# Kernel optimization log

Measured on AMD Instinct MI355X. Metric: run time of the kernel, lower is better.

The kernel has to match this reference:

```python
import jax, jax.numpy as jnp
import numpy as np

B, N, NC, DIM, H, D, M, TOPK = 1, 2048, 2048, 1024, 16, 64, 16, 64


def _l2norm(t):
    # F.normalize(t, p=2, dim=-1)
    return t / jnp.clip(jnp.linalg.norm(t, axis=-1, keepdims=True), 1e-12)


def _attn_layer(x, ctx, q_mask, k_mask, Wq, Wk, Wv, th_pre, th_post,
                mem_k, mem_v, scale_p, hs, Wo):
    b, n, _ = x.shape
    h, m, d = mem_k.shape
    nc = ctx.shape[1]
    q = (x @ Wq).reshape(b, n, h, d).transpose(0, 2, 1, 3)      # b h i d
    k = (ctx @ Wk).reshape(b, nc, h, d).transpose(0, 2, 1, 3)   # b h j d
    v = (ctx @ Wv).reshape(b, nc, h, d).transpose(0, 2, 1, 3)
    # memory key/values prepended
    k = jnp.concatenate([jnp.broadcast_to(mem_k[None], (b, h, m, d)), k], axis=2)
    v = jnp.concatenate([jnp.broadcast_to(mem_v[None], (b, h, m, d)), v], axis=2)
    # input mask (q_mask x k_mask), padded True over mem slots
    im = q_mask[:, None, :, None] & k_mask[:, None, None, :]    # b 1 i j
    im = jnp.pad(im, ((0, 0), (0, 0), (0, 0), (m, 0)), constant_values=True)
    # qk_norm: cosine-sim attention with learned per-head scale
    q = _l2norm(q)
    k = _l2norm(k)
    scale = 1.0 / jnp.clip(jnp.exp(scale_p), 0.01)              # [h]
    dots = jnp.einsum('bhid,bhjd->bhij', q, k) * scale[None, :, None, None]
    dots = jnp.einsum('gh,bhij->bgij', th_pre, dots)            # pre-softmax talking heads (1x1 conv over heads)
    neg = -jnp.finfo(dots.dtype).max
    dots = jnp.where(im, dots, neg)
    # sparse topk: keep only the TOPK largest logits per query
    kth = jax.lax.top_k(dots, TOPK)[0][..., -1:]
    dots = jnp.where(dots < kth, neg, dots)
    attn = jax.nn.softmax(dots, axis=-1)
    attn = jnp.einsum('gh,bhij->bgij', th_post, attn)           # post-softmax talking heads
    out = jnp.einsum('bhij,bhjd->bhid', attn, v)
    out = out * hs[None, :, None, None]                          # head scale
    out = out.transpose(0, 2, 1, 3).reshape(b, n, h * d)
    return out @ Wo


def setup_inputs():
    key = jax.random.key(0)
    ks = jax.random.split(key, 18)
    s = 1.0 / np.sqrt(DIM)
    sh = 1.0 / np.sqrt(H)

    def w(i, shape, scale=1.0):
        return jax.random.normal(ks[i], shape, dtype=jnp.float32) * scale

    return {
        'x': w(0, (B, N, DIM)),
        'context': w(1, (2, B, NC, DIM)),
        'mask': jnp.ones((B, N), dtype=bool),
        'context_mask': jnp.ones((B, NC), dtype=bool),
        'Wq1': w(2, (DIM, H * D), s), 'Wk1': w(3, (DIM, H * D), s), 'Wv1': w(4, (DIM, H * D), s),
        'Wq2': w(5, (DIM, H * D), s), 'Wk2': w(6, (DIM, H * D), s), 'Wv2': w(7, (DIM, H * D), s),
        'th_pre1': w(8, (H, H), sh), 'th_post1': w(9, (H, H), sh),
        'th_pre2': w(10, (H, H), sh), 'th_post2': w(11, (H, H), sh),
        'mem_k1': w(12, (H, M, D)), 'mem_v1': w(13, (H, M, D)),
        'mem_k2': w(14, (H, M, D)), 'mem_v2': w(15, (H, M, D)),
        'scale1': jnp.full((H,), -3.0, jnp.float32),
        'scale2': jnp.full((H,), -3.0, jnp.float32),
        'head_scale1': jnp.ones((H,), jnp.float32),
        'head_scale2': jnp.ones((H,), jnp.float32),
        'Wo1': w(16, (H * D, DIM), s), 'Wo2': w(17, (H * D, DIM), s),
    }


def reference(x, context, mask, context_mask,
              Wq1, Wk1, Wv1, Wq2, Wk2, Wv2,
              th_pre1, th_post1, th_pre2, th_post2,
              mem_k1, mem_v1, mem_k2, mem_v2,
              scale1, scale2, head_scale1, head_scale2, Wo1, Wo2):
    x = _attn_layer(x, context[0], mask, context_mask, Wq1, Wk1, Wv1,
                    th_pre1, th_post1, mem_k1, mem_v1, scale1, head_scale1, Wo1)
    x = _attn_layer(x, context[1], mask, context_mask, Wq2, Wk2, Wv2,
                    th_pre2, th_post2, mem_k2, mem_v2, scale2, head_scale2, Wo2)
    return x
```

## Files before the change

### kernel.cpp

```cpp
#include <hip/hip_runtime.h>

#define DEVI __device__ __forceinline__

typedef unsigned short u16;
typedef __attribute__((ext_vector_type(8))) _Float16 f16x8;
typedef __attribute__((ext_vector_type(4))) float f32x4;

#define NQ   2048
#define DIMM 1024
#define HD   16
#define MM   16
#define JTOT 2064
#define JPK  2080
#define JPAD 2112
#define KTOP 64

DEVI u16 f2h(float x) {
    _Float16 h = (_Float16)x;
    u16 r; __builtin_memcpy(&r, &h, 2); return r;
}
DEVI void fsplit(float x, u16& hi, u16& lo) {
    _Float16 h = (_Float16)x;
    float r = x - (float)h;
    _Float16 l = (_Float16)r;
    __builtin_memcpy(&hi, &h, 2);
    __builtin_memcpy(&lo, &l, 2);
}

__global__ __launch_bounds__(256) void split1_kernel(
    const float* __restrict__ s, u16* __restrict__ hi, u16* __restrict__ lo, int n4)
{
    int gid = blockIdx.x * 256 + threadIdx.x;
    if (gid < n4) {
        float4 v = ((const float4*)s)[gid];
        ushort4 h, l;
        fsplit(v.x, h.x, l.x); fsplit(v.y, h.y, l.y);
        fsplit(v.z, h.z, l.z); fsplit(v.w, h.w, l.w);
        ((ushort4*)hi)[gid] = h;
        ((ushort4*)lo)[gid] = l;
    }
}

struct P8 { const float* w[8]; };

__global__ __launch_bounds__(256) void wtrans_kernel(P8 src, u16* WTh, u16* WTl) {
    __shared__ float T[64][65];
    const float* W = src.w[blockIdx.z];
    size_t off = (size_t)blockIdx.z * DIMM * DIMM;
    int n0 = blockIdx.x * 64, k0 = blockIdx.y * 64;
#pragma unroll
    for (int rep = 0; rep < 16; ++rep) {
        int idx = rep * 256 + threadIdx.x;
        int kk = idx >> 6, nn = idx & 63;
        T[kk][nn] = W[(size_t)(k0 + kk) * DIMM + n0 + nn];
    }
    __syncthreads();
#pragma unroll
    for (int rep = 0; rep < 16; ++rep) {
        int idx = rep * 256 + threadIdx.x;
        int nn = idx >> 6, kk = idx & 63;
        u16 h, l; fsplit(T[kk][nn], h, l);
        WTh[off + (size_t)(n0 + nn) * DIMM + k0 + kk] = h;
        WTl[off + (size_t)(n0 + nn) * DIMM + k0 + kk] = l;
    }
}

template<int OM>
__global__ __launch_bounds__(256) void gemm_nt(
    const u16* __restrict__ A, int lda, long sA,
    const u16* __restrict__ B, int ldb, long sB,
    void* __restrict__ Cv, int ldc, long sC, int K)
{
    __shared__ u16 As[64 * 40];
    __shared__ u16 Bs[64 * 40];
    const int tid = threadIdx.x;
    const int z = blockIdx.z;
    A += (size_t)z * sA; B += (size_t)z * sB;
    const int bm = blockIdx.x * 64, bn = blockIdx.y * 64;
    const int l = tid & 63, w = tid >> 6;
    const int wm = (w >> 1) * 32, wn = (w & 1) * 32;
    const int srow = tid >> 2, skcol = (tid & 3) * 8;
    const u16* Ag = A + (size_t)(bm + srow) * lda + skcol;
    const u16* Bg = B + (size_t)(bn + srow) * ldb + skcol;
    const int lr = l & 15, lk = (l >> 4) * 8;
    f32x4 acc[2][2] = {};
    for (int k0 = 0; k0 < K; k0 += 32) {
        uint4 av = *(const uint4*)(Ag + k0);
        uint4 bv = *(const uint4*)(Bg + k0);
        __syncthreads();
        *(uint4*)&As[srow * 40 + skcol] = av;
        *(uint4*)&Bs[srow * 40 + skcol] = bv;
        __syncthreads();
        f16x8 a0 = *(const f16x8*)&As[(wm + lr) * 40 + lk];
        f16x8 a1 = *(const f16x8*)&As[(wm + 16 + lr) * 40 + lk];
        f16x8 b0 = *(const f16x8*)&Bs[(wn + lr) * 40 + lk];
        f16x8 b1 = *(const f16x8*)&Bs[(wn + 16 + lr) * 40 + lk];
        acc[0][0] = __builtin_amdgcn_mfma_f32_16x16x32_f16(a0, b0, acc[0][0], 0, 0, 0);
        acc[0][1] = __builtin_amdgcn_mfma_f32_16x16x32_f16(a0, b1, acc[0][1], 0, 0, 0);
        acc[1][0] = __builtin_amdgcn_mfma_f32_16x16x32_f16(a1, b0, acc[1][0], 0, 0, 0);
        acc[1][1] = __builtin_amdgcn_mfma_f32_16x16x32_f16(a1, b1, acc[1][1], 0, 0, 0);
    }
    const int crow0 = bm + wm + (l >> 4) * 4;
    const int ccol0 = bn + wn + lr;
#pragma unroll
    for (int mi = 0; mi < 2; ++mi)
#pragma unroll
        for (int ni = 0; ni < 2; ++ni)
#pragma unroll
            for (int r = 0; r < 4; ++r) {
                int row = crow0 + mi * 16 + r;
                int col = ccol0 + ni * 16;
                if (OM == 0) {
                    float* C = (float*)Cv + (size_t)z * sC;
                    C[(size_t)row * ldc + col] = acc[mi][ni][r];
                } else {
                    u16* C = (u16*)Cv + (size_t)z * sC;
                    C[(size_t)row * ldc + col] = f2h(acc[mi][ni][r]);
                }
            }
}

__global__ __launch_bounds__(256) void gemm3_nt(
    const u16* __restrict__ Ah, const u16* __restrict__ Al, int lda,
    const u16* __restrict__ Bh, const u16* __restrict__ Bl, int ldb,
    float* __restrict__ C, int ldc, int K)
{
    __shared__ u16 Ash[64 * 40];
    __shared__ u16 Asl[64 * 40];
    __shared__ u16 Bsh[64 * 40];
    __shared__ u16 Bsl[64 * 40];
    const int tid = threadIdx.x;
    const int bm = blockIdx.x * 64, bn = blockIdx.y * 64;
    const int l = tid & 63, w = tid >> 6;
    const int wm = (w >> 1) * 32, wn = (w & 1) * 32;
    const int srow = tid >> 2, skcol = (tid & 3) * 8;
    const size_t aoff = (size_t)(bm + srow) * lda + skcol;
    const size_t boff = (size_t)(bn + srow) * ldb + skcol;
    const int lr = l & 15, lk = (l >> 4) * 8;
    f32x4 acc[2][2] = {};
    for (int k0 = 0; k0 < K; k0 += 32) {
        uint4 avh = *(const uint4*)(Ah + aoff + k0);
        uint4 avl = *(const uint4*)(Al + aoff + k0);
        uint4 bvh = *(const uint4*)(Bh + boff + k0);
        uint4 bvl = *(const uint4*)(Bl + boff + k0);
        __syncthreads();
        *(uint4*)&Ash[srow * 40 + skcol] = avh;
        *(uint4*)&Asl[srow * 40 + skcol] = avl;
        *(uint4*)&Bsh[srow * 40 + skcol] = bvh;
        *(uint4*)&Bsl[srow * 40 + skcol] = bvl;
        __syncthreads();
        f16x8 a0h = *(const f16x8*)&Ash[(wm + lr) * 40 + lk];
        f16x8 a1h = *(const f16x8*)&Ash[(wm + 16 + lr) * 40 + lk];
        f16x8 a0l = *(const f16x8*)&Asl[(wm + lr) * 40 + lk];
        f16x8 a1l = *(const f16x8*)&Asl[(wm + 16 + lr) * 40 + lk];
        f16x8 b0h = *(const f16x8*)&Bsh[(wn + lr) * 40 + lk];
        f16x8 b1h = *(const f16x8*)&Bsh[(wn + 16 + lr) * 40 + lk];
        f16x8 b0l = *(const f16x8*)&Bsl[(wn + lr) * 40 + lk];
        f16x8 b1l = *(const f16x8*)&Bsl[(wn + 16 + lr) * 40 + lk];
#define MF(acc_, a_, b_) acc_ = __builtin_amdgcn_mfma_f32_16x16x32_f16(a_, b_, acc_, 0, 0, 0)
        MF(acc[0][0], a0h, b0h); MF(acc[0][0], a0h, b0l); MF(acc[0][0], a0l, b0h);
        MF(acc[0][1], a0h, b1h); MF(acc[0][1], a0h, b1l); MF(acc[0][1], a0l, b1h);
        MF(acc[1][0], a1h, b0h); MF(acc[1][0], a1h, b0l); MF(acc[1][0], a1l, b0h);
        MF(acc[1][1], a1h, b1h); MF(acc[1][1], a1h, b1l); MF(acc[1][1], a1l, b1h);
#undef MF
    }
    const int crow0 = bm + wm + (l >> 4) * 4;
    const int ccol0 = bn + wn + lr;
#pragma unroll
    for (int mi = 0; mi < 2; ++mi)
#pragma unroll
        for (int ni = 0; ni < 2; ++ni)
#pragma unroll
            for (int r = 0; r < 4; ++r)
                C[(size_t)(crow0 + mi * 16 + r) * ldc + ccol0 + ni * 16] = acc[mi][ni][r];
}

__global__ __launch_bounds__(256) void normq_kernel(
    const float* __restrict__ Qf, const float* __restrict__ scp,
    u16* __restrict__ qnh, u16* __restrict__ qnl)
{
    int w = threadIdx.x >> 6, l = threadIdx.x & 63;
    int wid = blockIdx.x * 4 + w;
    int h = wid >> 11, i = wid & 2047;
    float x = Qf[(size_t)i * DIMM + h * 64 + l];
    float ss = x * x;
#pragma unroll
    for (int m = 32; m; m >>= 1) ss += __shfl_xor(ss, m);
    float inv = 1.0f / fmaxf(sqrtf(ss), 1e-12f);
    float sc = 1.0f / fmaxf(expf(scp[h]), 0.01f);
    u16 hh, ll; fsplit(x * inv * sc, hh, ll);
    size_t idx = ((size_t)h * NQ + i) * 64 + l;
    qnh[idx] = hh; qnl[idx] = ll;
}

__global__ __launch_bounds__(256) void buildkn_kernel(
    const float* __restrict__ Kf, const float* __restrict__ mem_k,
    u16* __restrict__ knh, u16* __restrict__ knl)
{
    int w = threadIdx.x >> 6, l = threadIdx.x & 63;
    int wid = blockIdx.x * 4 + w;
    int h = wid / JPK, j = wid - h * JPK;
    float x = (j < MM) ? mem_k[((size_t)h * MM + j) * 64 + l]
            : (j < JTOT) ? Kf[(size_t)(j - MM) * DIMM + h * 64 + l] : 0.0f;
    float ss = x * x;
#pragma unroll
    for (int m = 32; m; m >>= 1) ss += __shfl_xor(ss, m);
    float inv = 1.0f / fmaxf(sqrtf(ss), 1e-12f);
    u16 hh, ll; fsplit(x * inv, hh, ll);
    size_t idx = ((size_t)h * JPK + j) * 64 + l;
    knh[idx] = hh; knl[idx] = ll;
}

__global__ __launch_bounds__(256) void buildvvT_kernel(
    const float* __restrict__ Vf, const float* __restrict__ mem_v,
    const float* __restrict__ hsp, u16* __restrict__ vvT)
{
    __shared__ float T[64][65];
    int h = blockIdx.z, j0 = blockIdx.x * 64;
    float hs = hsp[h];
#pragma unroll
    for (int rep = 0; rep < 16; ++rep) {
        int idx = rep * 256 + threadIdx.x;
        int jl = idx >> 6, d = idx & 63;
        int j = j0 + jl;
        float x = (j < MM) ? mem_v[((size_t)h * MM + j) * 64 + d]
                : (j < JTOT) ? Vf[(size_t)(j - MM) * DIMM + h * 64 + d] : 0.0f;
        T[jl][d] = x * hs;
    }
    __syncthreads();
#pragma unroll
    for (int rep = 0; rep < 16; ++rep) {
        int idx = rep * 256 + threadIdx.x;
        int d = idx >> 6, jl = idx & 63;
        vvT[((size_t)h * 64 + d) * JPAD + j0 + jl] = f2h(T[jl][d]);
    }
}

__global__ __launch_bounds__(256) void dots_kernel(
    const u16* __restrict__ qnh, const u16* __restrict__ qnl,
    const u16* __restrict__ knh, const u16* __restrict__ knl,
    const float* __restrict__ th_pre, float* __restrict__ D,
    int q0, int NQC)
{
    __shared__ float red[4][8][256];
    const int tid = threadIdx.x, l = tid & 63, w = tid >> 6;
    const int gx = gridDim.x, nwg = gx * gridDim.y;
    const int lin = blockIdx.y * gx + blockIdx.x;
    const int q8 = nwg >> 3, r8 = nwg & 7;
    const int xcd = lin & 7, idx8 = lin >> 3;
    const int swz = ((xcd < r8) ? xcd * (q8 + 1)
                                : r8 * (q8 + 1) + (xcd - r8) * q8) + idx8;
    const int it = (swz % gx) * 16;
    const int jt = (swz / gx) * 16;
    const int lr = l & 15, lk = (l >> 4) * 8;
    const int qrow = q0 + it + lr;
    const int jrow = jt + lr;
    f32x4 accg[16] = {};
#pragma unroll
    for (int hh = 0; hh < 4; ++hh) {
        const int h = w * 4 + hh;
        size_t qo = (((size_t)h * NQ + qrow) << 6) + lk;
        size_t ko = (((size_t)h * JPK + jrow) << 6) + lk;
        const f16x8* pah = (const f16x8*)(qnh + qo);
        const f16x8* pal = (const f16x8*)(qnl + qo);
        const f16x8* pbh = (const f16x8*)(knh + ko);
        const f16x8* pbl = (const f16x8*)(knl + ko);
        f16x8 a0h = pah[0], a1h = pah[4];
        f16x8 a0l = pal[0], a1l = pal[4];
        f16x8 b0h = pbh[0], b1h = pbh[4];
        f16x8 b0l = pbl[0], b1l = pbl[4];
        f32x4 ah = {};
        ah = __builtin_amdgcn_mfma_f32_16x16x32_f16(a0h, b0h, ah, 0, 0, 0);
        ah = __builtin_amdgcn_mfma_f32_16x16x32_f16(a1h, b1h, ah, 0, 0, 0);
        ah = __builtin_amdgcn_mfma_f32_16x16x32_f16(a0h, b0l, ah, 0, 0, 0);
        ah = __builtin_amdgcn_mfma_f32_16x16x32_f16(a1h, b1l, ah, 0, 0, 0);
        ah = __builtin_amdgcn_mfma_f32_16x16x32_f16(a0l, b0h, ah, 0, 0, 0);
        ah = __builtin_amdgcn_mfma_f32_16x16x32_f16(a1l, b1h, ah, 0, 0, 0);
#pragma unroll
        for (int g = 0; g < 16; ++g)
            accg[g] += th_pre[g * 16 + h] * ah;
    }
    const int orow = it + (l >> 4) * 4;
    const int col = jt + lr;
#pragma unroll
    for (int ph = 0; ph < 2; ++ph) {
        __syncthreads();
#pragma unroll
        for (int g = 0; g < 8; ++g)
            *(f32x4*)&red[w][g][l * 4] = accg[ph * 8 + g];
        __syncthreads();
#pragma unroll
        for (int gq = 0; gq < 2; ++gq) {
            const int gl = w * 2 + gq;
            f32x4 s = *(const f32x4*)&red[0][gl][l * 4];
            s += *(const f32x4*)&red[1][gl][l * 4];
            s += *(const f32x4*)&red[2][gl][l * 4];
            s += *(const f32x4*)&red[3][gl][l * 4];
            const int g = ph * 8 + gl;
#pragma unroll
            for (int r = 0; r < 4; ++r)
                D[((size_t)(orow + r) * 16 + g) * JPAD + col] = s[r];
        }
    }
}

__global__ __launch_bounds__(256) void estats_kernel(
    const float* __restrict__ D, u16* __restrict__ E)
{
    const int w = threadIdx.x >> 6, l = threadIdx.x & 63;
    const int r = blockIdx.x * 4 + w;
    const float* Dr = D + (size_t)r * JPAD;
    float v[33]; unsigned ku[33];
#pragma unroll
    for (int s = 0; s < 33; ++s) {
        int j = s * 64 + l;
        float x = (j < JTOT) ? Dr[j] : -3.0e38f;
        v[s] = x;
        unsigned u = __float_as_uint(x);
        ku[s] = (j < JTOT) ? ((u & 0x80000000u) ? ~u : (u | 0x80000000u)) : 0u;
    }
    unsigned t = 0;
    for (int b = 31; b >= 0; --b) {
        unsigned tc = t | (1u << b);
        int c = 0;
#pragma unroll
        for (int s = 0; s < 33; ++s)
            c += (int)__popcll(__ballot(ku[s] >= tc));
        if (c >= KTOP) t = tc;
    }
    float mx = v[0];
#pragma unroll
    for (int s = 1; s < 33; ++s) mx = fmaxf(mx, v[s]);
#pragma unroll
    for (int m = 32; m; m >>= 1) mx = fmaxf(mx, __shfl_xor(mx, m));
    float den = 0.0f;
#pragma unroll
    for (int s = 0; s < 33; ++s) {
        float ev = (ku[s] >= t) ? __expf(v[s] - mx) : 0.0f;
        v[s] = ev; den += ev;
    }
#pragma unroll
    for (int m = 32; m; m >>= 1) den += __shfl_xor(den, m);
    float inv = 1.0f / den;
    u16* Er = E + (size_t)r * JPAD;
#pragma unroll
    for (int s = 0; s < 33; ++s)
        Er[s * 64 + l] = f2h(v[s] * inv);
}

__global__ __launch_bounds__(256) void mixp_kernel(
    const u16* __restrict__ E, const float* __restrict__ th_post,
    u16* __restrict__ P)
{
    const int tid = threadIdx.x, l = tid & 63, w = tid >> 6;
    const int i = blockIdx.x, by = blockIdx.y;
    const int g = l & 15, hg = l >> 4, hb = (hg & 1) * 8;
    f16x8 afr;
#pragma unroll
    for (int idx = 0; idx < 8; ++idx) {
        int k = hg * 8 + idx;
        afr[idx] = (_Float16)((k < 16) ? th_post[g * 16 + k] : 0.0f);
    }
    const u16* Eb = E + (size_t)i * 16 * JPAD;
    u16* Pb = P + (size_t)i * 16 * JPAD;
    for (int t = by * 4 + w; t < 129; t += 16) {
        const int j = t * 16 + g;
        f16x8 bfr;
#pragma unroll
        for (int idx = 0; idx < 8; ++idx) {
            u16 raw = Eb[(size_t)(hb + idx) * JPAD + j];
            _Float16 hv; __builtin_memcpy(&hv, &raw, 2);
            bfr[idx] = hv;
        }
        f32x4 c = {};
        c = __builtin_amdgcn_mfma_f32_16x16x32_f16(afr, bfr, c, 0, 0, 0);
#pragma unroll
        for (int r = 0; r < 4; ++r)
            Pb[(size_t)(hg * 4 + r) * JPAD + j] = f2h(c[r]);
    }
}

extern "C" void kernel_launch(void* const* d_in, const int* in_sizes, int n_in,
                              void* d_out, int out_size, void* d_ws, size_t ws_size,
                              hipStream_t stream)
{
    (void)in_sizes; (void)n_in; (void)out_size;
    const float* x      = (const float*)d_in[0];
    const float* ctx    = (const float*)d_in[1];
    const float* Wq1    = (const float*)d_in[4];
    const float* Wk1    = (const float*)d_in[5];
    const float* Wv1    = (const float*)d_in[6];
    const float* Wq2    = (const float*)d_in[7];
    const float* Wk2    = (const float*)d_in[8];
    const float* Wv2    = (const float*)d_in[9];
    const float* thpre1 = (const float*)d_in[10];
    const float* thpost1= (const float*)d_in[11];
    const float* thpre2 = (const float*)d_in[12];
    const float* thpost2= (const float*)d_in[13];
    const float* memk1  = (const float*)d_in[14];
    const float* memv1  = (const float*)d_in[15];
    const float* memk2  = (const float*)d_in[16];
    const float* memv2  = (const float*)d_in[17];
    const float* sc1    = (const float*)d_in[18];
    const float* sc2    = (const float*)d_in[19];
    const float* hs1    = (const float*)d_in[20];
    const float* hs2    = (const float*)d_in[21];
    const float* Wo1    = (const float*)d_in[22];
    const float* Wo2    = (const float*)d_in[23];

    char* p = (char*)d_ws;
    auto alloc = [&](size_t n) { char* r = p; p += (n + 255) & ~(size_t)255; return r; };
    u16*   xbh   = (u16*)alloc((size_t)NQ * DIMM * 2);
    u16*   xbl   = (u16*)alloc((size_t)NQ * DIMM * 2);
    u16*   cb0h  = (u16*)alloc((size_t)NQ * DIMM * 2);
    u16*   cb0l  = (u16*)alloc((size_t)NQ * DIMM * 2);
    u16*   cb1h  = (u16*)alloc((size_t)NQ * DIMM * 2);
    u16*   cb1l  = (u16*)alloc((size_t)NQ * DIMM * 2);
    u16*   WTh   = (u16*)alloc((size_t)8 * DIMM * DIMM * 2);
    u16*   WTl   = (u16*)alloc((size_t)8 * DIMM * DIMM * 2);
    float* Qf    = (float*)alloc((size_t)NQ * DIMM * 4);
    float* Kf    = (float*)alloc((size_t)NQ * DIMM * 4);
    float* Vf    = (float*)alloc((size_t)NQ * DIMM * 4);
    u16*   qnh   = (u16*)alloc((size_t)16 * NQ * 64 * 2);
    u16*   qnl   = (u16*)alloc((size_t)16 * NQ * 64 * 2);
    u16*   knh   = (u16*)alloc((size_t)16 * JPK * 64 * 2);
    u16*   knl   = (u16*)alloc((size_t)16 * JPK * 64 * 2);
    u16*   vvT   = (u16*)alloc((size_t)16 * 64 * JPAD * 2);
    u16*   attnA = (u16*)alloc((size_t)NQ * DIMM * 2);
    size_t used = (size_t)(p - (char*)d_ws);

    int NQC = 32;
    for (int cand : {512, 256, 128, 64}) {
        if (used + (size_t)16 * cand * JPAD * 8 + 1024 <= ws_size) { NQC = cand; break; }
    }
    float* Dbuf = (float*)alloc((size_t)16 * NQC * JPAD * 4);
    u16*   Ebuf = (u16*)alloc((size_t)16 * NQC * JPAD * 2);
    u16*   Pbuf = (u16*)alloc((size_t)16 * NQC * JPAD * 2);

    const int N4 = (NQ * DIMM) / 4;
    split1_kernel<<<2048, 256, 0, stream>>>(x, xbh, xbl, N4);
    split1_kernel<<<2048, 256, 0, stream>>>(ctx, cb0h, cb0l, N4);
    split1_kernel<<<2048, 256, 0, stream>>>(ctx + (size_t)NQ * DIMM, cb1h, cb1l, N4);
    P8 w8{ { Wq1, Wk1, Wv1, Wo1, Wq2, Wk2, Wv2, Wo2 } };
    wtrans_kernel<<<dim3(16, 16, 8), 256, 0, stream>>>(w8, WTh, WTl);

    auto layer = [&](const u16* inh, const u16* inl,
                     const u16* ctxh, const u16* ctxl, int wbase,
                     const float* thpre, const float* thpost,
                     const float* memk, const float* memv,
                     const float* scp, const float* hsp, int li) {
        size_t o_q = (size_t)(wbase + 0) * DIMM * DIMM;
        size_t o_k = (size_t)(wbase + 1) * DIMM * DIMM;
        size_t o_v = (size_t)(wbase + 2) * DIMM * DIMM;
        size_t o_o = (size_t)(wbase + 3) * DIMM * DIMM;
        gemm3_nt<<<dim3(32, 16), 256, 0, stream>>>(inh, inl, DIMM, WTh + o_q, WTl + o_q, DIMM, Qf, DIMM, DIMM);
        gemm3_nt<<<dim3(32, 16), 256, 0, stream>>>(ctxh, ctxl, DIMM, WTh + o_k, WTl + o_k, DIMM, Kf, DIMM, DIMM);
        gemm_nt<0><<<dim3(32, 16, 1), 256, 0, stream>>>(ctxh, DIMM, 0, WTh + o_v, DIMM, 0, Vf, DIMM, 0, DIMM);
        normq_kernel<<<(16 * NQ) / 4, 256, 0, stream>>>(Qf, scp, qnh, qnl);
        buildkn_kernel<<<(16 * JPK) / 4, 256, 0, stream>>>(Kf, memk, knh, knl);
        buildvvT_kernel<<<dim3(33, 1, 16), 256, 0, stream>>>(Vf, memv, hsp, vvT);
        int nch = NQ / NQC;
        for (int c = 0; c < nch; ++c) {
            int q0 = c * NQC;
            dots_kernel<<<dim3(NQC / 16, JTOT / 16), 256, 0, stream>>>(qnh, qnl, knh, knl, thpre, Dbuf, q0, NQC);
            estats_kernel<<<(16 * NQC) / 4, 256, 0, stream>>>(Dbuf, Ebuf);
            mixp_kernel<<<dim3(NQC, 4), 256, 0, stream>>>(Ebuf, thpost, Pbuf);
            gemm_nt<1><<<dim3(NQC / 64, 1, 16), 256, 0, stream>>>(
                Pbuf, 16 * JPAD, (long)JPAD, vvT, JPAD, (long)64 * JPAD,
                attnA + (size_t)q0 * DIMM, DIMM, 64, JPAD);
        }
        if (li == 0) {
            gemm_nt<0><<<dim3(32, 16, 1), 256, 0, stream>>>(attnA, DIMM, 0, WTh + o_o, DIMM, 0, Qf, DIMM, 0, DIMM);
            split1_kernel<<<2048, 256, 0, stream>>>(Qf, xbh, xbl, N4);
        } else {
            gemm_nt<0><<<dim3(32, 16, 1), 256, 0, stream>>>(attnA, DIMM, 0, WTh + o_o, DIMM, 0, d_out, DIMM, 0, DIMM);
        }
    };

    layer(xbh, xbl, cb0h, cb0l, 0, thpre1, thpost1, memk1, memv1, sc1, hs1, 0);
    layer(xbh, xbl, cb1h, cb1l, 4, thpre2, thpost2, memk2, memv2, sc2, hs2, 1);
}
```

Before: 1.575 ms.

## Split talking-heads pre-mix into separate MFMA kernel and enlarge query chunks

The dots kernel now writes per-head similarity scores as split fp16 hi/lo pairs instead of doing the 16x16 head mixing with scalar FMAs and an LDS reduction. A new premix kernel reloads those scores and applies th_pre through 3-term split-fp16 MFMAs into the float D buffer. The chunk-size search now allows whole-sequence chunks (up to 2048 queries), which cuts launch count. In exchange it adds an extra global round trip of the score tensor and an additional kernel launch per chunk.

```diff
diff --git a/kernel.cpp b/kernel.cpp
--- a/kernel.cpp
+++ b/kernel.cpp
@@ -239,10 +239,8 @@
 __global__ __launch_bounds__(256) void dots_kernel(
     const u16* __restrict__ qnh, const u16* __restrict__ qnl,
     const u16* __restrict__ knh, const u16* __restrict__ knl,
-    const float* __restrict__ th_pre, float* __restrict__ D,
-    int q0, int NQC)
-{
-    __shared__ float red[4][8][256];
+    u16* __restrict__ Sh, u16* __restrict__ Sl, int q0)
+{
     const int tid = threadIdx.x, l = tid & 63, w = tid >> 6;
     const int gx = gridDim.x, nwg = gx * gridDim.y;
     const int lin = blockIdx.y * gx + blockIdx.x;
@@ -255,7 +253,8 @@
     const int lr = l & 15, lk = (l >> 4) * 8;
     const int qrow = q0 + it + lr;
     const int jrow = jt + lr;
-    f32x4 accg[16] = {};
+    const int orow = it + (l >> 4) * 4;
+    const int col = jt + lr;
 #pragma unroll
     for (int hh = 0; hh < 4; ++hh) {
         const int h = w * 4 + hh;
@@ -277,30 +276,51 @@
         ah = __builtin_amdgcn_mfma_f32_16x16x32_f16(a0l, b0h, ah, 0, 0, 0);
         ah = __builtin_amdgcn_mfma_f32_16x16x32_f16(a1l, b1h, ah, 0, 0, 0);
 #pragma unroll
-        for (int g = 0; g < 16; ++g)
-            accg[g] += th_pre[g * 16 + h] * ah;
-    }
-    const int orow = it + (l >> 4) * 4;
-    const int col = jt + lr;
-#pragma unroll
-    for (int ph = 0; ph < 2; ++ph) {
-        __syncthreads();
-#pragma unroll
-        for (int g = 0; g < 8; ++g)
-            *(f32x4*)&red[w][g][l * 4] = accg[ph * 8 + g];
-        __syncthreads();
-#pragma unroll
-        for (int gq = 0; gq < 2; ++gq) {
-            const int gl = w * 2 + gq;
-            f32x4 s = *(const f32x4*)&red[0][gl][l * 4];
-            s += *(const f32x4*)&red[1][gl][l * 4];
-            s += *(const f32x4*)&red[2][gl][l * 4];
-            s += *(const f32x4*)&red[3][gl][l * 4];
-            const int g = ph * 8 + gl;
-#pragma unroll
-            for (int r = 0; r < 4; ++r)
-                D[((size_t)(orow + r) * 16 + g) * JPAD + col] = s[r];
+        for (int r = 0; r < 4; ++r) {
+            u16 hi16, lo16; fsplit(ah[r], hi16, lo16);
+            size_t off = ((size_t)(orow + r) * 16 + h) * JPAD + col;
+            Sh[off] = hi16; Sl[off] = lo16;
         }
+    }
+}
+
+__global__ __launch_bounds__(256) void premix_kernel(
+    const u16* __restrict__ Sh, const u16* __restrict__ Sl,
+    const float* __restrict__ th_pre, float* __restrict__ D)
+{
+    const int tid = threadIdx.x, l = tid & 63, w = tid >> 6;
+    const int i = blockIdx.x, by = blockIdx.y;
+    const int g = l & 15, hg = l >> 4, hb = (hg & 1) * 8;
+    f16x8 ah, al;
+#pragma unroll
+    for (int idx = 0; idx < 8; ++idx) {
+        int k = hg * 8 + idx;
+        float v = (k < 16) ? th_pre[g * 16 + k] : 0.0f;
+        _Float16 vh = (_Float16)v;
+        ah[idx] = vh;
+        al[idx] = (_Float16)(v - (float)vh);
+    }
+    const u16* Shb = Sh + (size_t)i * 16 * JPAD;
+    const u16* Slb = Sl + (size_t)i * 16 * JPAD;
+    float* Db = D + (size_t)i * 16 * JPAD;
+    for (int t = by * 4 + w; t < 129; t += 16) {
+        const int j = t * 16 + g;
+        f16x8 bh, bl;
+#pragma unroll
+        for (int idx = 0; idx < 8; ++idx) {
+            u16 rh = Shb[(size_t)(hb + idx) * JPAD + j];
+            u16 rl = Slb[(size_t)(hb + idx) * JPAD + j];
+            _Float16 h1, h2;
+            __builtin_memcpy(&h1, &rh, 2); __builtin_memcpy(&h2, &rl, 2);
+            bh[idx] = h1; bl[idx] = h2;
+        }
+        f32x4 c = {};
+        c = __builtin_amdgcn_mfma_f32_16x16x32_f16(ah, bh, c, 0, 0, 0);
+        c = __builtin_amdgcn_mfma_f32_16x16x32_f16(ah, bl, c, 0, 0, 0);
+        c = __builtin_amdgcn_mfma_f32_16x16x32_f16(al, bh, c, 0, 0, 0);
+#pragma unroll
+        for (int r = 0; r < 4; ++r)
+            Db[(size_t)(hg * 4 + r) * JPAD + j] = c[r];
     }
 }
 
@@ -430,12 +450,14 @@
     size_t used = (size_t)(p - (char*)d_ws);
 
     int NQC = 32;
-    for (int cand : {512, 256, 128, 64}) {
-        if (used + (size_t)16 * cand * JPAD * 8 + 1024 <= ws_size) { NQC = cand; break; }
+    for (int cand : {2048, 1024, 512, 256, 128, 64}) {
+        if (used + (size_t)16 * cand * JPAD * 12 + 4096 <= ws_size) { NQC = cand; break; }
     }
     float* Dbuf = (float*)alloc((size_t)16 * NQC * JPAD * 4);
     u16*   Ebuf = (u16*)alloc((size_t)16 * NQC * JPAD * 2);
     u16*   Pbuf = (u16*)alloc((size_t)16 * NQC * JPAD * 2);
+    u16*   Shb  = (u16*)alloc((size_t)16 * NQC * JPAD * 2);
+    u16*   Slb  = (u16*)alloc((size_t)16 * NQC * JPAD * 2);
 
     const int N4 = (NQ * DIMM) / 4;
     split1_kernel<<<2048, 256, 0, stream>>>(x, xbh, xbl, N4);
@@ -462,7 +484,8 @@
         int nch = NQ / NQC;
         for (int c = 0; c < nch; ++c) {
             int q0 = c * NQC;
-            dots_kernel<<<dim3(NQC / 16, JTOT / 16), 256, 0, stream>>>(qnh, qnl, knh, knl, thpre, Dbuf, q0, NQC);
+            dots_kernel<<<dim3(NQC / 16, JTOT / 16), 256, 0, stream>>>(qnh, qnl, knh, knl, Shb, Slb, q0);
+            premix_kernel<<<dim3(NQC, 4), 256, 0, stream>>>(Shb, Slb, thpre, Dbuf);
             estats_kernel<<<(16 * NQC) / 4, 256, 0, stream>>>(Dbuf, Ebuf);
             mixp_kernel<<<dim3(NQC, 4), 256, 0, stream>>>(Ebuf, thpost, Pbuf);
             gemm_nt<1><<<dim3(NQC / 64, 1, 16), 256, 0, stream>>>(
```

New measurement: 2.127 ms. 35.0% more time.
